# Optimization experiments

Hardware: AMD Instinct MI355X
Metric: run time of the kernel (lower is better)

The kernel has to match this reference:

```python
import jax, jax.numpy as jnp
import numpy as np

F = 128          # feature_dim
EMB = 128        # emb_dim[i] (all equal)
GH = 4           # gat heads per conv
GD = EMB // GH   # per-head conv out dim (is_concat=True)
AH = 8           # num_agg_heads
HID = EMB // AH  # n_hidden = 16
R = 3            # num_relations
L = 2            # num_layers
NC = 2           # num_classes
N = [100000, 50000, 25000]   # src frontier sizes per block (dst of block i = N[i+1])
E = [500000, 250000]         # edges per relation per block
SLOPE_CONV = 0.2             # DGL GATConv leaky slope
SLOPE_ACT = 0.01             # nn.LeakyReLU default

def lrelu(x, s):
    return jnp.where(x >= 0, x, s * x)

def setup_inputs() -> dict:
    key = jax.random.key(0)
    ks = iter(jax.random.split(key, 64))
    d = {}
    d['x'] = jax.random.normal(next(ks), (N[0], F), jnp.float32)
    d['src0'] = jax.random.randint(next(ks), (R, E[0]), 0, N[0], jnp.int32)
    d['dst0'] = jax.random.randint(next(ks), (R, E[0]), 0, N[1], jnp.int32)
    d['src1'] = jax.random.randint(next(ks), (R, E[1]), 0, N[1], jnp.int32)
    d['dst1'] = jax.random.randint(next(ks), (R, E[1]), 0, N[2], jnp.int32)
    def p(shape):
        return jax.random.normal(next(ks), shape, jnp.float32) * 0.05
    d['conv_W'] = p((L, R, F, EMB)); d['conv_al'] = p((L, R, GH, GD)); d['conv_ar'] = p((L, R, GH, GD))
    d['feat_W'] = p((L, F, EMB)); d['feat_b'] = p((L, EMB))
    d['relWl_W'] = p((L, F, EMB)); d['relWl_b'] = p((L, EMB))
    d['relWr_W'] = p((L, EMB, EMB)); d['relWr_b'] = p((L, EMB))
    d['relP_W'] = p((L, EMB, EMB)); d['relP_b'] = p((L, EMB))
    d['rela_W'] = p((L, HID)); d['rela_b'] = p((L,))
    d['proj_W'] = p((F, EMB)); d['proj_b'] = p((EMB,))
    d['hopWl_W'] = p((F, EMB)); d['hopWl_b'] = p((EMB,))
    d['hopWr_W'] = p((EMB, EMB)); d['hopWr_b'] = p((EMB,))
    d['hopP_W'] = p((EMB, EMB)); d['hopP_b'] = p((EMB,))
    d['hopa_W'] = p((HID,)); d['hopa_b'] = p(())
    d['lin_W'] = p((EMB, NC)); d['lin_b'] = p((NC,))
    return d

def gat_conv(x, n_dst, src, dst, W, al, ar):
    # x: [N_src, in]; dst features are x[:n_dst] (DGL block convention)
    h = (x @ W).reshape(-1, GH, GD)                 # [N_src, GH, GD]
    el = jnp.sum(h * al, -1)                        # [N_src, GH]
    er = jnp.sum(h * ar, -1)
    e = lrelu(el[src] + er[dst], SLOPE_CONV)        # [E, GH]
    emax = jax.ops.segment_max(e, dst, num_segments=n_dst)
    ee = jnp.exp(e - emax[dst])
    den = jax.ops.segment_sum(ee, dst, num_segments=n_dst)
    a = ee / den[dst]                               # edge softmax per dst node
    out = jax.ops.segment_sum(a[:, :, None] * h[src], dst, num_segments=n_dst)
    return out.reshape(n_dst, EMB)                  # is_concat reshape

def gated_attn(prev, feats, Wl, bl, Wr, br, Wp, bp, aW, ab):
    # prev: [n, in]; feats: [n, k, EMB]
    n, k, _ = feats.shape
    gl = (prev @ Wl + bl).reshape(n, AH, HID)
    gr = (feats @ Wr + br).reshape(n, k, AH, HID)
    z = lrelu(gl[:, None] + gr, SLOPE_ACT)
    e = jnp.einsum('nkah,h->nka', z, aW) + ab       # [n, k, AH]
    a = jax.nn.softmax(e, axis=1)                   # shift-invariant, matches e - amax
    v = (feats @ Wp + bp).reshape(n, k, AH, HID)
    return jnp.einsum('nka,nkah->nah', a, v).reshape(n, EMB)

def reference(x, src0, dst0, src1, dst1, conv_W, conv_al, conv_ar, feat_W, feat_b,
              relWl_W, relWl_b, relWr_W, relWr_b, relP_W, relP_b, rela_W, rela_b,
              proj_W, proj_b, hopWl_W, hopWl_b, hopWr_W, hopWr_b, hopP_W, hopP_b,
              hopa_W, hopa_b, lin_W, lin_b):
    n_out = N[L]
    layer_features = [x[:n_out] @ proj_W + proj_b]
    h = x
    srcs = [src0, src1]; dsts = [dst0, dst1]
    for i in range(L):
        n_dst = N[i + 1]
        feats = [lrelu(gat_conv(h, n_dst, srcs[i][j], dsts[i][j],
                                conv_W[i, j], conv_al[i, j], conv_ar[i, j]), SLOPE_ACT)
                 for j in range(R)]
        x_dst = h[:n_dst]
        feats.append(lrelu(x_dst @ feat_W[i] + feat_b[i], SLOPE_ACT))
        stacked = jnp.stack(feats, 1)               # [n_dst, R+1, EMB]
        h = lrelu(gated_attn(x_dst, stacked, relWl_W[i], relWl_b[i], relWr_W[i],
                             relWr_b[i], relP_W[i], relP_b[i], rela_W[i], rela_b[i]),
                  SLOPE_ACT)
        layer_features.append(h[:n_out])
    stacked = jnp.stack(layer_features, 1)          # [n_out, L+1, EMB]
    out = lrelu(gated_attn(x[:n_out], stacked, hopWl_W, hopWl_b, hopWr_W, hopWr_b,
                           hopP_W, hopP_b, hopa_W, hopa_b), SLOPE_ACT)
    return out @ lin_W + lin_b                      # [n_out, NC]
```

## Files before the change

### kernel.cpp

```cpp
#include <hip/hip_runtime.h>

#define N0 100000
#define N1 50000
#define N2 25000
#define E0 500000
#define E1 250000
#define N_TOT (3 * N1 + 3 * N2)
#define NE_ALL (3 * E0 + 3 * E1)
#define BNODE 512
#define NBUCK ((N_TOT + BNODE - 1) / BNODE)
#define BCAP 12288

typedef __attribute__((ext_vector_type(8))) short short8;
typedef __attribute__((ext_vector_type(4))) float f32x4;
typedef unsigned short ushort_t;
typedef unsigned int uint_t;

static __device__ __forceinline__ float lrelu(float x, float s) {
    return x >= 0.f ? x : s * x;
}

static __device__ __forceinline__ ushort_t f2bf(float f) {
    union { float f; uint_t u; } v; v.f = f;
    uint_t r = v.u + 0x7FFFu + ((v.u >> 16) & 1u);
    return (ushort_t)(r >> 16);
}

static __device__ __forceinline__ float bf_lo(uint_t u) {
    union { uint_t i; float f; } v; v.i = u << 16;
    return v.f;
}
static __device__ __forceinline__ float bf_hi(uint_t u) {
    union { uint_t i; float f; } v; v.i = u & 0xFFFF0000u;
    return v.f;
}

static __device__ __forceinline__ uint_t cvt2(float lo, float hi) {
    uint_t r;
    asm("v_cvt_pk_bf16_f32 %0, %1, %2" : "=v"(r) : "v"(lo), "v"(hi));
    return r;
}

template <int CT, int PLANES, int OUTMODE, int AB16, int OB16 = 0, int REPY = 0>
__global__ __launch_bounds__(256) void gemm_bf16(
    const void* __restrict__ A0, const void* __restrict__ A1,
    const void* __restrict__ A2, const void* __restrict__ A3,
    int nodes, const ushort_t* __restrict__ Bt, int cols,
    const float* __restrict__ biasA, const float* __restrict__ biasB,
    int colsplit, float slopeA, float slopeB,
    void* __restrict__ O1, int ld1, float* __restrict__ O2, int ld2,
    const float* __restrict__ glp, const float* __restrict__ aWp, int kreal,
    int repB = 0, int repO1 = 0, int repO2 = 0)
{
    constexpr int BCOLS = CT * 16;
    constexpr int NPANEL = (OUTMODE == 4) ? 2 : 1;
    constexpr int SCOLS = BCOLS * NPANEL;
    constexpr int CSTR = BCOLS + 4;
    constexpr int SH_B = SCOLS * 256;
    constexpr int SH_C = 64 * CSTR * 4 + ((OUTMODE == 4) ? 2048 : 0);
    constexpr int SHSZ = SH_B > SH_C ? SH_B : SH_C;
    constexpr int AELT = AB16 ? 2 : 4;
    __shared__ char sh[SHSZ];
    float* Cs = (float*)sh;

    const int Mrows = nodes * PLANES;
    const int row0 = blockIdx.x * 128;
    const int repy = REPY ? blockIdx.y : 0;
    const int cbase = REPY ? 0 : blockIdx.y * BCOLS;
    const ushort_t* Btp = Bt + (REPY ? (size_t)repy * repB : 0);
    ushort_t* O1p = (ushort_t*)O1 + (REPY ? (size_t)repy * repO1 : 0);
    float* O2p = O2 + (REPY ? (size_t)repy * repO2 : 0);
    const int tid = threadIdx.x;

    for (int u = tid; u < SCOLS * 16; u += 256) {
        int cl = u >> 4;
        int q = u & 15;
        int off = cl * 256 + q * 16;
        off ^= (cl & 7) << 4;
        int c;
        if (OUTMODE == 4)
            c = (cl < BCOLS) ? (cbase + cl) : (128 + cbase + (cl - BCOLS));
        else
            c = cbase + cl;
        uint4 d = make_uint4(0, 0, 0, 0);
        if (c < cols) d = *(const uint4*)(Btp + (size_t)c * 128 + q * 8);
        *(uint4*)(sh + off) = d;
    }
    __syncthreads();

    const int wv = tid >> 6;
    const int l = tid & 63;
    const int kg = l >> 4;
    const char* aptr[2];
    #pragma unroll
    for (int rt = 0; rt < 2; ++rt) {
        int rg = row0 + wv * 32 + rt * 16 + (l & 15);
        if (rg >= Mrows) rg = Mrows - 1;
        int node, pl;
        if (PLANES == 1) { node = rg; pl = 0; }
        else { node = rg / PLANES; pl = rg % PLANES; }
        const void* base = (pl == 0) ? A0 : (pl == 1) ? A1 : (pl == 2) ? A2 : A3;
        aptr[rt] = (const char*)base + ((size_t)node * 128 + kg * 8) * AELT;
    }

    f32x4 acc[2][CT];
    f32x4 accV[2][(OUTMODE == 4) ? CT : 1];
    #pragma unroll
    for (int a = 0; a < 2; ++a) {
        #pragma unroll
        for (int b = 0; b < CT; ++b)
            #pragma unroll
            for (int q = 0; q < 4; ++q) acc[a][b][q] = 0.f;
        if (OUTMODE == 4)
            #pragma unroll
            for (int b = 0; b < CT; ++b)
                #pragma unroll
                for (int q = 0; q < 4; ++q) accV[a][b][q] = 0.f;
    }

    #pragma unroll
    for (int kt = 0; kt < 4; ++kt) {
        short8 af[2];
        #pragma unroll
        for (int rt = 0; rt < 2; ++rt) {
            if (AB16) {
                af[rt] = *(const short8*)(aptr[rt] + (size_t)kt * 64);
            } else {
                const float4* p = (const float4*)(aptr[rt] + (size_t)kt * 128);
                float4 x0 = p[0];
                float4 x1 = p[1];
                union { uint_t u[4]; short8 s; } u;
                u.u[0] = cvt2(x0.x, x0.y);
                u.u[1] = cvt2(x0.z, x0.w);
                u.u[2] = cvt2(x1.x, x1.y);
                u.u[3] = cvt2(x1.z, x1.w);
                af[rt] = u.s;
            }
        }
        #pragma unroll
        for (int ct = 0; ct < CT; ++ct) {
            int off = ((ct * 16 + (l & 15)) * 256) + kt * 64 + (l >> 4) * 16;
            off ^= (l & 7) << 4;
            short8 bfr = *(const short8*)(sh + off);
            acc[0][ct] = __builtin_amdgcn_mfma_f32_16x16x32_bf16(af[0], bfr, acc[0][ct], 0, 0, 0);
            acc[1][ct] = __builtin_amdgcn_mfma_f32_16x16x32_bf16(af[1], bfr, acc[1][ct], 0, 0, 0);
            if (OUTMODE == 4) {
                int offv = ((BCOLS + ct * 16 + (l & 15)) * 256) + kt * 64 + (l >> 4) * 16;
                offv ^= (l & 7) << 4;
                short8 bfv = *(const short8*)(sh + offv);
                accV[0][ct] = __builtin_amdgcn_mfma_f32_16x16x32_bf16(af[0], bfv, accV[0][ct], 0, 0, 0);
                accV[1][ct] = __builtin_amdgcn_mfma_f32_16x16x32_bf16(af[1], bfv, accV[1][ct], 0, 0, 0);
            }
        }
    }

    if (OUTMODE == 4) {
        const int node0 = row0 >> 2;
        float* e_sh = (float*)(sh + 64 * CSTR * 4);
        float* w_sh = e_sh + 256;
        float4 aw0 = ((const float4*)aWp)[0];
        float4 aw1 = ((const float4*)aWp)[1];
        float4 aw2 = ((const float4*)aWp)[2];
        float4 aw3 = ((const float4*)aWp)[3];
        #pragma unroll
        for (int rt = 0; rt < 2; ++rt) {
            __syncthreads();
            #pragma unroll
            for (int ct = 0; ct < CT; ++ct) {
                int col = ct * 16 + (l & 15);
                float br_ = biasA[cbase + col];
                int lrow = wv * 16 + (l >> 4) * 4;
                #pragma unroll
                for (int j = 0; j < 4; ++j)
                    Cs[(lrow + j) * CSTR + col] = acc[rt][ct][j] + br_;
            }
            __syncthreads();
            {
                int row = tid >> 2, head = tid & 3;
                int rg = row0 + ((row >> 4) << 5) + rt * 16 + (row & 15);
                int node = rg >> 2;
                if (node > nodes - 1) node = nodes - 1;
                const float* zr = &Cs[row * CSTR + head * 16];
                const float* glr = glp + (size_t)node * 128 + cbase + head * 16;
                float4 c0 = *(const float4*)(zr);
                float4 c1 = *(const float4*)(zr + 4);
                float4 c2 = *(const float4*)(zr + 8);
                float4 c3 = *(const float4*)(zr + 12);
                float4 g0 = *(const float4*)(glr);
                float4 g1 = *(const float4*)(glr + 4);
                float4 g2 = *(const float4*)(glr + 8);
                float4 g3 = *(const float4*)(glr + 12);
                float e =
                    lrelu(c0.x + g0.x, 0.01f) * aw0.x + lrelu(c0.y + g0.y, 0.01f) * aw0.y +
                    lrelu(c0.z + g0.z, 0.01f) * aw0.z + lrelu(c0.w + g0.w, 0.01f) * aw0.w +
                    lrelu(c1.x + g1.x, 0.01f) * aw1.x + lrelu(c1.y + g1.y, 0.01f) * aw1.y +
                    lrelu(c1.z + g1.z, 0.01f) * aw1.z + lrelu(c1.w + g1.w, 0.01f) * aw1.w +
                    lrelu(c2.x + g2.x, 0.01f) * aw2.x + lrelu(c2.y + g2.y, 0.01f) * aw2.y +
                    lrelu(c2.z + g2.z, 0.01f) * aw2.z + lrelu(c2.w + g2.w, 0.01f) * aw2.w +
                    lrelu(c3.x + g3.x, 0.01f) * aw3.x + lrelu(c3.y + g3.y, 0.01f) * aw3.y +
                    lrelu(c3.z + g3.z, 0.01f) * aw3.z + lrelu(c3.w + g3.w, 0.01f) * aw3.w;
                e_sh[row * 4 + head] = e;
            }
            __syncthreads();
            if (tid < 64) {
                int q = tid >> 2, head = tid & 3;
                int rho0 = (q >> 2) * 16 + (q & 3) * 4;
                float e0 = e_sh[(rho0 + 0) * 4 + head];
                float e1 = e_sh[(rho0 + 1) * 4 + head];
                float e2 = e_sh[(rho0 + 2) * 4 + head];
                float e3 = (kreal == 4) ? e_sh[(rho0 + 3) * 4 + head] : -1e30f;
                float m = fmaxf(fmaxf(e0, e1), fmaxf(e2, e3));
                float x0 = __expf(e0 - m), x1 = __expf(e1 - m), x2 = __expf(e2 - m);
                float x3 = (kreal == 4) ? __expf(e3 - m) : 0.f;
                float inv = 1.f / (x0 + x1 + x2 + x3);
                w_sh[q * 16 + 0 + head] = x0 * inv;
                w_sh[q * 16 + 4 + head] = x1 * inv;
                w_sh[q * 16 + 8 + head] = x2 * inv;
                w_sh[q * 16 + 12 + head] = x3 * inv;
            }
            __syncthreads();
            #pragma unroll
            for (int ct = 0; ct < CT; ++ct) {
                int col = ct * 16 + (l & 15);
                float bp_ = biasB[cbase + col];
                int lrow = wv * 16 + (l >> 4) * 4;
                #pragma unroll
                for (int j = 0; j < 4; ++j)
                    Cs[(lrow + j) * CSTR + col] = accV[rt][ct][j] + bp_;
            }
            __syncthreads();
            {
                int nidx = tid >> 4;
                int c4 = tid & 15;
                int nl = rt * 4 + (nidx >> 2) * 8 + (nidx & 3);
                int gn = node0 + nl;
                if (gn < nodes) {
                    int head = c4 >> 2;
                    float4 o = make_float4(0.f, 0.f, 0.f, 0.f);
                    #pragma unroll
                    for (int k = 0; k < 4; ++k) {
                        int rho = (nidx >> 2) * 16 + (nidx & 3) * 4 + k;
                        float wk = w_sh[nidx * 16 + k * 4 + head];
                        float4 v4 = *(const float4*)&Cs[rho * CSTR + c4 * 4];
                        o.x += wk * v4.x; o.y += wk * v4.y;
                        o.z += wk * v4.z; o.w += wk * v4.w;
                    }
                    o.x = lrelu(o.x, 0.01f); o.y = lrelu(o.y, 0.01f);
                    o.z = lrelu(o.z, 0.01f); o.w = lrelu(o.w, 0.01f);
                    if (OB16) {
                        uint2 pk;
                        pk.x = cvt2(o.x, o.y);
                        pk.y = cvt2(o.z, o.w);
                        *(uint2*)((ushort_t*)O1 + (size_t)gn * 128 + cbase + c4 * 4) = pk;
                    } else {
                        *(float4*)((float*)O1 + (size_t)gn * 128 + cbase + c4 * 4) = o;
                    }
                }
            }
        }
        return;
    }

    #pragma unroll
    for (int rt = 0; rt < 2; ++rt) {
        __syncthreads();
        #pragma unroll
        for (int ct = 0; ct < CT; ++ct) {
            int c = cbase + ct * 16 + (l & 15);
            float bias_ = 0.f, slope_ = 1.f;
            if (c < colsplit) {
                if (biasA) bias_ = biasA[c];
                slope_ = slopeA;
            } else if (c < cols) {
                if (biasB) bias_ = biasB[c - colsplit];
                slope_ = slopeB;
            }
            int lrow = wv * 16 + (l >> 4) * 4;
            #pragma unroll
            for (int j = 0; j < 4; ++j) {
                float v = acc[rt][ct][j] + bias_;
                v = v >= 0.f ? v : v * slope_;
                Cs[(lrow + j) * CSTR + ct * 16 + (l & 15)] = v;
            }
        }
        __syncthreads();
        for (int i = tid; i < 64 * CT * 4; i += 256) {
            int rho = i / (CT * 4);
            int c4 = i - rho * (CT * 4);
            int col = c4 * 4;
            int gcol = cbase + col;
            int rg = row0 + rt * 16 + (rho >> 4) * 32 + (rho & 15);
            if (rg >= Mrows || gcol >= cols) continue;
            float4 v = *(const float4*)&Cs[rho * CSTR + col];
            if (gcol < 128) {
                uint2 pk;
                pk.x = cvt2(v.x, v.y);
                pk.y = cvt2(v.z, v.w);
                *(uint2*)(O1p + (size_t)rg * ld1 + gcol) = pk;
            } else {
                *(float4*)(O2p + (size_t)rg * ld2 + (gcol - 128)) = v;
            }
        }
    }
}

__global__ __launch_bounds__(256) void cvt_bf16(
    const float* __restrict__ in, ushort_t* __restrict__ out, int n8)
{
    int i = blockIdx.x * 256 + threadIdx.x;
    if (i >= n8) return;
    const float4* p = (const float4*)(in + (size_t)i * 8);
    float4 a = p[0], b = p[1];
    uint4 pk;
    pk.x = cvt2(a.x, a.y); pk.y = cvt2(a.z, a.w);
    pk.z = cvt2(b.x, b.y); pk.w = cvt2(b.z, b.w);
    *(uint4*)(out + (size_t)i * 8) = pk;
}

__global__ __launch_bounds__(128) void prep2(
    const float* __restrict__ Wa, const float* __restrict__ Wb, ushort_t* __restrict__ dst)
{
    int c = blockIdx.x, k = threadIdx.x;
    const float* W = (c < 128) ? Wa : Wb;
    int cc = c & 127;
    dst[c * 128 + k] = f2bf(W[k * 128 + cc]);
}

__global__ __launch_bounds__(128) void prep_conv(
    const float* __restrict__ W, const float* __restrict__ al, const float* __restrict__ ar,
    ushort_t* __restrict__ dst)
{
    int c = blockIdx.x, k = threadIdx.x;
    float v;
    if (c < 128) {
        v = W[k * 128 + c];
    } else {
        int idx = c - 128;
        int g = idx & 3;
        const float* a = (idx < 4) ? al : ar;
        float s = 0.f;
        for (int d = 0; d < 32; ++d) s += W[k * 128 + g * 32 + d] * a[g * 32 + d];
        v = s;
    }
    dst[c * 128 + k] = f2bf(v);
}

static __device__ __forceinline__ void edge_decode(
    int idx, const int* __restrict__ src0, const int* __restrict__ dst0,
    const int* __restrict__ src1, const int* __restrict__ dst1,
    int& src, int& gnode)
{
    if (idx < 3 * E0) {
        src = src0[idx];
        gnode = (idx / E0) * N1 + dst0[idx];
    } else {
        int k = idx - 3 * E0;
        src = src1[k];
        gnode = 3 * N1 + (k / E1) * N2 + dst1[k];
    }
}

__global__ __launch_bounds__(256) void bin_pass(
    const int* __restrict__ src0, const int* __restrict__ dst0,
    const int* __restrict__ src1, const int* __restrict__ dst1,
    int* __restrict__ bcur, uint_t* __restrict__ tmp)
{
    __shared__ int lcnt[512];
    __shared__ int lbase[512];
    const int tid = threadIdx.x;
    const int e0 = blockIdx.x * 4096;
    int sv[16], gv[16];
    for (int t = tid; t < 512; t += 256) lcnt[t] = 0;
    __syncthreads();
    #pragma unroll
    for (int i = 0; i < 16; ++i) {
        int idx = e0 + i * 256 + tid;
        if (idx < NE_ALL) {
            edge_decode(idx, src0, dst0, src1, dst1, sv[i], gv[i]);
            atomicAdd(&lcnt[gv[i] >> 9], 1);
        } else {
            gv[i] = -1; sv[i] = 0;
        }
    }
    __syncthreads();
    for (int t = tid; t < 512; t += 256) {
        int c = lcnt[t];
        lbase[t] = c ? atomicAdd(&bcur[t], c) : 0;
        lcnt[t] = 0;
    }
    __syncthreads();
    #pragma unroll
    for (int i = 0; i < 16; ++i) {
        if (gv[i] >= 0) {
            int b = gv[i] >> 9;
            int p = lbase[b] + atomicAdd(&lcnt[b], 1);
            if (p < BCAP)
                tmp[(size_t)b * BCAP + p] = (uint_t)((sv[i] << 9) | (gv[i] & 511));
        }
    }
}

__global__ __launch_bounds__(512) void bucket_scan(
    const int* __restrict__ bcur, int* __restrict__ bbase)
{
    __shared__ int s[512];
    int t = threadIdx.x;
    int v = (t < NBUCK) ? bcur[t] : 0;
    s[t] = v;
    __syncthreads();
    for (int off = 1; off < 512; off <<= 1) {
        int x = (t >= off) ? s[t - off] : 0;
        __syncthreads();
        s[t] += x;
        __syncthreads();
    }
    bbase[t] = s[t] - v;
}

__global__ __launch_bounds__(256) void build_pass(
    const int* __restrict__ bcur, const int* __restrict__ bbase,
    const uint_t* __restrict__ tmp, int* __restrict__ offs, int* __restrict__ csr)
{
    __shared__ int cnt[512];
    __shared__ int offl[512];
    __shared__ int ps[256];
    const int tid = threadIdx.x;
    const int b = blockIdx.x;
    int nE = bcur[b];
    if (nE > BCAP) nE = BCAP;
    const int base = bbase[b];
    const int node0 = b * BNODE;
    const uint_t* tp = tmp + (size_t)b * BCAP;

    for (int t = tid; t < 512; t += 256) cnt[t] = 0;
    __syncthreads();
    for (int i = tid; i < nE; i += 256)
        atomicAdd(&cnt[tp[i] & 511], 1);
    __syncthreads();
    int a0 = cnt[2 * tid], a1 = cnt[2 * tid + 1];
    ps[tid] = a0 + a1;
    __syncthreads();
    for (int off = 1; off < 256; off <<= 1) {
        int x = (tid >= off) ? ps[tid - off] : 0;
        __syncthreads();
        ps[tid] += x;
        __syncthreads();
    }
    int ex = ps[tid] - (a0 + a1);
    offl[2 * tid] = ex;
    offl[2 * tid + 1] = ex + a0;
    __syncthreads();
    for (int t = tid; t < BNODE; t += 256) {
        int gn = node0 + t;
        if (gn < N_TOT) offs[gn] = base + offl[t];
    }
    if (b == NBUCK - 1 && tid == 0) offs[N_TOT] = base + nE;
    for (int t = tid; t < 512; t += 256) cnt[t] = 0;
    __syncthreads();
    for (int i = tid; i < nE; i += 256) {
        uint_t pk = tp[i];
        int ld = pk & 511;
        int p = atomicAdd(&cnt[ld], 1);
        csr[base + offl[ld] + p] = (int)(pk >> 9);
    }
}

__global__ __launch_bounds__(256) void gat_gather6(
    const int* __restrict__ csrc, const int* __restrict__ offs,
    int base0, int nPerRep,
    const float* __restrict__ elr, int elrStride,
    const ushort_t* __restrict__ P, int pStride,
    ushort_t* __restrict__ out, int outStride)
{
    const int wv = threadIdx.x >> 6;
    const int g = blockIdx.x * 4 + wv;
    if (g >= 3 * nPerRep) return;
    const int rep = g / nPerRep;
    const int node = g - rep * nPerRep;
    const float* elrp = elr + (size_t)rep * elrStride;
    const ushort_t* Pp = P + (size_t)rep * pStride;
    ushort_t* outp = out + (size_t)rep * outStride;

    const int l = threadIdx.x & 63;
    const uint_t lane16 = l & 15;
    const int slot = l >> 4;
    const uint_t hg = lane16 >> 2;
    const int beg = offs[base0 + g], end = offs[base0 + g + 1];
    const float erg = elrp[(uint_t)node * 8u + 4u + hg];
    float den = 0.f;
    float a0 = 0.f, a1 = 0.f, a2 = 0.f, a3 = 0.f;
    float a4 = 0.f, a5 = 0.f, a6 = 0.f, a7 = 0.f;
    int i = beg + slot;
    for (; i + 4 < end; i += 8) {
        uint_t s0 = (uint_t)csrc[i];
        uint_t s1 = (uint_t)csrc[i + 4];
        float w0 = __expf(lrelu(elrp[s0 * 8u + hg] + erg, 0.2f));
        float w1 = __expf(lrelu(elrp[s1 * 8u + hg] + erg, 0.2f));
        uint4 d0 = *(const uint4*)(Pp + s0 * 128u + lane16 * 8u);
        uint4 d1 = *(const uint4*)(Pp + s1 * 128u + lane16 * 8u);
        den += w0 + w1;
        a0 += w0 * bf_lo(d0.x) + w1 * bf_lo(d1.x);
        a1 += w0 * bf_hi(d0.x) + w1 * bf_hi(d1.x);
        a2 += w0 * bf_lo(d0.y) + w1 * bf_lo(d1.y);
        a3 += w0 * bf_hi(d0.y) + w1 * bf_hi(d1.y);
        a4 += w0 * bf_lo(d0.z) + w1 * bf_lo(d1.z);
        a5 += w0 * bf_hi(d0.z) + w1 * bf_hi(d1.z);
        a6 += w0 * bf_lo(d0.w) + w1 * bf_lo(d1.w);
        a7 += w0 * bf_hi(d0.w) + w1 * bf_hi(d1.w);
    }
    if (i < end) {
        uint_t s0 = (uint_t)csrc[i];
        float w0 = __expf(lrelu(elrp[s0 * 8u + hg] + erg, 0.2f));
        uint4 d0 = *(const uint4*)(Pp + s0 * 128u + lane16 * 8u);
        den += w0;
        a0 += w0 * bf_lo(d0.x); a1 += w0 * bf_hi(d0.x);
        a2 += w0 * bf_lo(d0.y); a3 += w0 * bf_hi(d0.y);
        a4 += w0 * bf_lo(d0.z); a5 += w0 * bf_hi(d0.z);
        a6 += w0 * bf_lo(d0.w); a7 += w0 * bf_hi(d0.w);
    }
    #pragma unroll
    for (int m = 16; m <= 32; m <<= 1) {
        den += __shfl_xor(den, m);
        a0 += __shfl_xor(a0, m); a1 += __shfl_xor(a1, m);
        a2 += __shfl_xor(a2, m); a3 += __shfl_xor(a3, m);
        a4 += __shfl_xor(a4, m); a5 += __shfl_xor(a5, m);
        a6 += __shfl_xor(a6, m); a7 += __shfl_xor(a7, m);
    }
    if (slot == 0) {
        float inv = (end > beg) ? 1.f / den : 0.f;
        uint4 pk;
        pk.x = cvt2(lrelu(a0 * inv, 0.01f), lrelu(a1 * inv, 0.01f));
        pk.y = cvt2(lrelu(a2 * inv, 0.01f), lrelu(a3 * inv, 0.01f));
        pk.z = cvt2(lrelu(a4 * inv, 0.01f), lrelu(a5 * inv, 0.01f));
        pk.w = cvt2(lrelu(a6 * inv, 0.01f), lrelu(a7 * inv, 0.01f));
        *(uint4*)(outp + (uint_t)node * 128u + lane16 * 8u) = pk;
    }
}

__global__ __launch_bounds__(256) void lin_kernel(
    const float* __restrict__ H, const float* __restrict__ W,
    const float* __restrict__ b, float* __restrict__ out, int n)
{
    int idx = blockIdx.x * 256 + threadIdx.x;
    int node = idx >> 1, c = idx & 1;
    if (node >= n) return;
    float acc = 0.f;
    for (int k = 0; k < 128; ++k)
        acc += H[(size_t)node * 128 + k] * W[k * 2 + c];
    out[(size_t)node * 2 + c] = acc + b[c];
}

extern "C" void kernel_launch(void* const* d_in, const int* in_sizes, int n_in,
                              void* d_out, int out_size, void* d_ws, size_t ws_size,
                              hipStream_t stream)
{
    (void)in_sizes; (void)n_in; (void)out_size; (void)ws_size;
    const float* x       = (const float*)d_in[0];
    const int*   src0    = (const int*)d_in[1];
    const int*   dst0    = (const int*)d_in[2];
    const int*   src1    = (const int*)d_in[3];
    const int*   dst1    = (const int*)d_in[4];
    const float* conv_W  = (const float*)d_in[5];
    const float* conv_al = (const float*)d_in[6];
    const float* conv_ar = (const float*)d_in[7];
    const float* feat_W  = (const float*)d_in[8];
    const float* feat_b  = (const float*)d_in[9];
    const float* relWl_W = (const float*)d_in[10];
    const float* relWl_b = (const float*)d_in[11];
    const float* relWr_W = (const float*)d_in[12];
    const float* relWr_b = (const float*)d_in[13];
    const float* relP_W  = (const float*)d_in[14];
    const float* relP_b  = (const float*)d_in[15];
    const float* rela_W  = (const float*)d_in[16];
    const float* proj_W  = (const float*)d_in[18];
    const float* proj_b  = (const float*)d_in[19];
    const float* hopWl_W = (const float*)d_in[20];
    const float* hopWl_b = (const float*)d_in[21];
    const float* hopWr_W = (const float*)d_in[22];
    const float* hopWr_b = (const float*)d_in[23];
    const float* hopP_W  = (const float*)d_in[24];
    const float* hopP_b  = (const float*)d_in[25];
    const float* hopa_W  = (const float*)d_in[26];
    const float* lin_W   = (const float*)d_in[28];
    const float* lin_b   = (const float*)d_in[29];
    float* out = (float*)d_out;

    char* base = (char*)d_ws;
    size_t off = 0;
    auto alloc = [&](size_t bytes) -> void* {
        void* p = base + off;
        off += (bytes + 255) & ~(size_t)255;
        return p;
    };
    ushort_t* P     = (ushort_t*)alloc((size_t)3 * N0 * 128 * 2);
    float* elr      = (float*)alloc((size_t)3 * N0 * 8 * 4);
    ushort_t* x16   = (ushort_t*)alloc((size_t)N0 * 128 * 2);
    ushort_t* F     = (ushort_t*)alloc((size_t)3 * N1 * 128 * 2);
    ushort_t* F3    = (ushort_t*)alloc((size_t)N1 * 128 * 2);
    ushort_t* h1    = (ushort_t*)alloc((size_t)N1 * 128 * 2);
    ushort_t* h2    = (ushort_t*)alloc((size_t)N2 * 128 * 2);
    float* glbuf    = (float*)alloc((size_t)N1 * 128 * 4);
    float* glhop    = (float*)alloc((size_t)N2 * 128 * 4);
    int*   csr_all  = (int*)alloc((size_t)NE_ALL * 4);
    int*   offs     = (int*)alloc((size_t)(N_TOT + 1) * 4);
    int*   bcur     = (int*)alloc(512 * 4);
    int*   bbase    = (int*)alloc(512 * 4);
    ushort_t* pconvA = (ushort_t*)alloc((size_t)6 * 136 * 128 * 2);
    ushort_t* p2L0 = (ushort_t*)alloc(256 * 128 * 2);
    ushort_t* p2L1 = (ushort_t*)alloc(256 * 128 * 2);
    ushort_t* pE   = (ushort_t*)alloc(256 * 128 * 2);
    ushort_t* pF0  = (ushort_t*)alloc(256 * 128 * 2);
    ushort_t* pF1  = (ushort_t*)alloc(256 * 128 * 2);
    ushort_t* pG   = (ushort_t*)alloc(256 * 128 * 2);

    ushort_t* F0 = F;
    ushort_t* F1 = F + (size_t)N1 * 128;
    ushort_t* F2 = F + (size_t)2 * N1 * 128;
    ushort_t* hopp0 = F0;
    float* hout  = glbuf;
    uint_t* tmp  = (uint_t*)F;

    for (int i = 0; i < 6; ++i)
        prep_conv<<<136, 128, 0, stream>>>(conv_W + (size_t)i * 16384,
                                           conv_al + (size_t)i * 128,
                                           conv_ar + (size_t)i * 128,
                                           pconvA + (size_t)i * 136 * 128);
    prep2<<<256, 128, 0, stream>>>(feat_W, relWl_W, p2L0);
    prep2<<<256, 128, 0, stream>>>(feat_W + 16384, relWl_W + 16384, p2L1);
    prep2<<<256, 128, 0, stream>>>(proj_W, hopWl_W, pE);
    prep2<<<256, 128, 0, stream>>>(relWr_W, relP_W, pF0);
    prep2<<<256, 128, 0, stream>>>(relWr_W + 16384, relP_W + 16384, pF1);
    prep2<<<256, 128, 0, stream>>>(hopWr_W, hopP_W, pG);
    cvt_bf16<<<(N0 * 16 + 255) / 256, 256, 0, stream>>>(x, x16, N0 * 16);

    hipMemsetAsync(bcur, 0, 512 * 4, stream);
    bin_pass<<<(NE_ALL + 4095) / 4096, 256, 0, stream>>>(src0, dst0, src1, dst1, bcur, tmp);
    bucket_scan<<<1, 512, 0, stream>>>(bcur, bbase);
    build_pass<<<NBUCK, 256, 0, stream>>>(bcur, bbase, tmp, offs, csr_all);

    gemm_bf16<9, 1, 1, 1, 0, 1><<<dim3((N0 + 127) / 128, 3), 256, 0, stream>>>(
        x16, x16, x16, x16, N0, pconvA, 136, nullptr, nullptr, 128, 1.f, 1.f,
        P, 128, elr, 8, nullptr, nullptr, 0,
        136 * 128, N0 * 128, N0 * 8);
    gat_gather6<<<(3 * N1 + 3) / 4, 256, 0, stream>>>(
        csr_all, offs, 0, N1, elr, N0 * 8, P, N0 * 128, F, N1 * 128);
    gemm_bf16<8, 1, 1, 1><<<dim3((N1 + 127) / 128, 2), 256, 0, stream>>>(
        x16, x16, x16, x16, N1, p2L0, 256, feat_b, relWl_b, 128, 0.01f, 1.f,
        F3, 128, glbuf, 128, nullptr, nullptr, 0);
    gemm_bf16<4, 4, 4, 1, 1><<<dim3((N1 * 4 + 127) / 128, 2), 256, 0, stream>>>(
        F0, F1, F2, F3, N1, pF0, 256, relWr_b, relP_b, 128, 1.f, 1.f,
        h1, 128, nullptr, 0, glbuf, rela_W, 4);

    gemm_bf16<9, 1, 1, 1, 0, 1><<<dim3((N1 + 127) / 128, 3), 256, 0, stream>>>(
        h1, h1, h1, h1, N1, pconvA + (size_t)3 * 136 * 128, 136,
        nullptr, nullptr, 128, 1.f, 1.f,
        P, 128, elr, 8, nullptr, nullptr, 0,
        136 * 128, N0 * 128, N0 * 8);
    gat_gather6<<<(3 * N2 + 3) / 4, 256, 0, stream>>>(
        csr_all, offs, 3 * N1, N2, elr, N0 * 8, P, N0 * 128, F, N1 * 128);
    gemm_bf16<8, 1, 1, 1><<<dim3((N2 + 127) / 128, 2), 256, 0, stream>>>(
        h1, h1, h1, h1, N2, p2L1, 256, feat_b + 128, relWl_b + 128, 128, 0.01f, 1.f,
        F3, 128, glbuf, 128, nullptr, nullptr, 0);
    gemm_bf16<4, 4, 4, 1, 1><<<dim3((N2 * 4 + 127) / 128, 2), 256, 0, stream>>>(
        F0, F1, F2, F3, N2, pF1, 256, relWr_b + 128, relP_b + 128, 128, 1.f, 1.f,
        h2, 128, nullptr, 0, glbuf, rela_W + 16, 4);

    gemm_bf16<8, 1, 1, 1><<<dim3((N2 + 127) / 128, 2), 256, 0, stream>>>(
        x16, x16, x16, x16, N2, pE, 256, proj_b, hopWl_b, 128, 1.f, 1.f,
        hopp0, 128, glhop, 128, nullptr, nullptr, 0);

    gemm_bf16<4, 4, 4, 1, 0><<<dim3((N2 * 4 + 127) / 128, 2), 256, 0, stream>>>(
        hopp0, h1, h2, hopp0, N2, pG, 256, hopWr_b, hopP_b, 128, 1.f, 1.f,
        hout, 128, nullptr, 0, glhop, hopa_W, 3);

    lin_kernel<<<(N2 * 2 + 255) / 256, 256, 0, stream>>>(hout, lin_W, lin_b, out, N2);
}
```

Before: 463.8 us.

## Merge prep launches, fold bucket scan into build pass, unroll gather by four

Thirteen weight-prep and input-cast launches are merged into one prep_all kernel dispatched by block index. The separate single-block bucket scan is removed; each build_pass block now recomputes the prefix sum over bucket counts itself. The GAT gather loop gets a four-edge unrolled path ahead of the two-edge loop to expose more memory-level parallelism. Together these cut launch count and gap overhead, at the cost of redundant scans per block and more registers in the gather.

```diff
diff --git a/kernel.cpp b/kernel.cpp
--- a/kernel.cpp
+++ b/kernel.cpp
@@ -304,45 +304,50 @@
     }
 }
 
-__global__ __launch_bounds__(256) void cvt_bf16(
-    const float* __restrict__ in, ushort_t* __restrict__ out, int n8)
+struct P2Job { const float* Wa; const float* Wb; ushort_t* dst; };
+struct PrepArgs {
+    const float* conv_W; const float* conv_al; const float* conv_ar;
+    ushort_t* pconvA;
+    P2Job j[6];
+    const float* x; ushort_t* x16;
+};
+
+__global__ __launch_bounds__(128) void prep_all(PrepArgs pa)
 {
-    int i = blockIdx.x * 256 + threadIdx.x;
-    if (i >= n8) return;
-    const float4* p = (const float4*)(in + (size_t)i * 8);
-    float4 a = p[0], b = p[1];
-    uint4 pk;
-    pk.x = cvt2(a.x, a.y); pk.y = cvt2(a.z, a.w);
-    pk.z = cvt2(b.x, b.y); pk.w = cvt2(b.z, b.w);
-    *(uint4*)(out + (size_t)i * 8) = pk;
-}
-
-__global__ __launch_bounds__(128) void prep2(
-    const float* __restrict__ Wa, const float* __restrict__ Wb, ushort_t* __restrict__ dst)
-{
-    int c = blockIdx.x, k = threadIdx.x;
-    const float* W = (c < 128) ? Wa : Wb;
-    int cc = c & 127;
-    dst[c * 128 + k] = f2bf(W[k * 128 + cc]);
-}
-
-__global__ __launch_bounds__(128) void prep_conv(
-    const float* __restrict__ W, const float* __restrict__ al, const float* __restrict__ ar,
-    ushort_t* __restrict__ dst)
-{
-    int c = blockIdx.x, k = threadIdx.x;
-    float v;
-    if (c < 128) {
-        v = W[k * 128 + c];
+    const int bid = blockIdx.x;
+    const int k = threadIdx.x;
+    if (bid < 816) {
+        int jj = bid / 136, c = bid - jj * 136;
+        const float* W = pa.conv_W + (size_t)jj * 16384;
+        float v;
+        if (c < 128) {
+            v = W[k * 128 + c];
+        } else {
+            int idx = c - 128;
+            int g = idx & 3;
+            const float* a = ((idx < 4) ? pa.conv_al : pa.conv_ar) + jj * 128;
+            float s = 0.f;
+            for (int d = 0; d < 32; ++d) s += W[k * 128 + g * 32 + d] * a[g * 32 + d];
+            v = s;
+        }
+        pa.pconvA[(size_t)jj * 136 * 128 + c * 128 + k] = f2bf(v);
+    } else if (bid < 816 + 1536) {
+        int b2 = bid - 816;
+        int jj = b2 >> 8, c = b2 & 255;
+        const float* W = (c < 128) ? pa.j[jj].Wa : pa.j[jj].Wb;
+        int cc = c & 127;
+        pa.j[jj].dst[c * 128 + k] = f2bf(W[k * 128 + cc]);
     } else {
-        int idx = c - 128;
-        int g = idx & 3;
-        const float* a = (idx < 4) ? al : ar;
-        float s = 0.f;
-        for (int d = 0; d < 32; ++d) s += W[k * 128 + g * 32 + d] * a[g * 32 + d];
-        v = s;
-    }
-    dst[c * 128 + k] = f2bf(v);
+        int idx = (bid - 2352) * 128 + k;
+        if (idx < N0 * 16) {
+            const float4* p = (const float4*)(pa.x + (size_t)idx * 8);
+            float4 a = p[0], b = p[1];
+            uint4 pk;
+            pk.x = cvt2(a.x, a.y); pk.y = cvt2(a.z, a.w);
+            pk.z = cvt2(b.x, b.y); pk.w = cvt2(b.z, b.w);
+            *(uint4*)(pa.x16 + (size_t)idx * 8) = pk;
+        }
+    }
 }
 
 static __device__ __forceinline__ void edge_decode(
@@ -400,45 +405,20 @@
     }
 }
 
-__global__ __launch_bounds__(512) void bucket_scan(
-    const int* __restrict__ bcur, int* __restrict__ bbase)
-{
-    __shared__ int s[512];
-    int t = threadIdx.x;
-    int v = (t < NBUCK) ? bcur[t] : 0;
-    s[t] = v;
-    __syncthreads();
-    for (int off = 1; off < 512; off <<= 1) {
-        int x = (t >= off) ? s[t - off] : 0;
-        __syncthreads();
-        s[t] += x;
-        __syncthreads();
-    }
-    bbase[t] = s[t] - v;
-}
-
-__global__ __launch_bounds__(256) void build_pass(
-    const int* __restrict__ bcur, const int* __restrict__ bbase,
-    const uint_t* __restrict__ tmp, int* __restrict__ offs, int* __restrict__ csr)
+__global__ __launch_bounds__(256) void build_pass2(
+    const int* __restrict__ bcur, const uint_t* __restrict__ tmp,
+    int* __restrict__ offs, int* __restrict__ csr)
 {
     __shared__ int cnt[512];
     __shared__ int offl[512];
     __shared__ int ps[256];
+    __shared__ int pbase[512];
     const int tid = threadIdx.x;
     const int b = blockIdx.x;
-    int nE = bcur[b];
-    if (nE > BCAP) nE = BCAP;
-    const int base = bbase[b];
-    const int node0 = b * BNODE;
-    const uint_t* tp = tmp + (size_t)b * BCAP;
-
-    for (int t = tid; t < 512; t += 256) cnt[t] = 0;
-    __syncthreads();
-    for (int i = tid; i < nE; i += 256)
-        atomicAdd(&cnt[tp[i] & 511], 1);
-    __syncthreads();
-    int a0 = cnt[2 * tid], a1 = cnt[2 * tid + 1];
-    ps[tid] = a0 + a1;
+
+    int v0 = (2 * tid < NBUCK) ? bcur[2 * tid] : 0;
+    int v1 = (2 * tid + 1 < NBUCK) ? bcur[2 * tid + 1] : 0;
+    ps[tid] = v0 + v1;
     __syncthreads();
     for (int off = 1; off < 256; off <<= 1) {
         int x = (tid >= off) ? ps[tid - off] : 0;
@@ -446,6 +426,33 @@
         ps[tid] += x;
         __syncthreads();
     }
+    {
+        int ex = ps[tid] - (v0 + v1);
+        pbase[2 * tid] = ex;
+        pbase[2 * tid + 1] = ex + v0;
+    }
+    __syncthreads();
+    const int base = pbase[b];
+
+    int nE = bcur[b];
+    if (nE > BCAP) nE = BCAP;
+    const int node0 = b * BNODE;
+    const uint_t* tp = tmp + (size_t)b * BCAP;
+
+    for (int t = tid; t < 512; t += 256) cnt[t] = 0;
+    __syncthreads();
+    for (int i = tid; i < nE; i += 256)
+        atomicAdd(&cnt[tp[i] & 511], 1);
+    __syncthreads();
+    int a0 = cnt[2 * tid], a1 = cnt[2 * tid + 1];
+    ps[tid] = a0 + a1;
+    __syncthreads();
+    for (int off = 1; off < 256; off <<= 1) {
+        int x = (tid >= off) ? ps[tid - off] : 0;
+        __syncthreads();
+        ps[tid] += x;
+        __syncthreads();
+    }
     int ex = ps[tid] - (a0 + a1);
     offl[2 * tid] = ex;
     offl[2 * tid + 1] = ex + a0;
@@ -465,7 +472,7 @@
     }
 }
 
-__global__ __launch_bounds__(256) void gat_gather6(
+__global__ __launch_bounds__(256) void gat_gather7(
     const int* __restrict__ csrc, const int* __restrict__ offs,
     int base0, int nPerRep,
     const float* __restrict__ elr, int elrStride,
@@ -491,6 +498,29 @@
     float a0 = 0.f, a1 = 0.f, a2 = 0.f, a3 = 0.f;
     float a4 = 0.f, a5 = 0.f, a6 = 0.f, a7 = 0.f;
     int i = beg + slot;
+    for (; i + 12 < end; i += 16) {
+        uint_t s0 = (uint_t)csrc[i];
+        uint_t s1 = (uint_t)csrc[i + 4];
+        uint_t s2 = (uint_t)csrc[i + 8];
+        uint_t s3 = (uint_t)csrc[i + 12];
+        float w0 = __expf(lrelu(elrp[s0 * 8u + hg] + erg, 0.2f));
+        float w1 = __expf(lrelu(elrp[s1 * 8u + hg] + erg, 0.2f));
+        float w2 = __expf(lrelu(elrp[s2 * 8u + hg] + erg, 0.2f));
+        float w3 = __expf(lrelu(elrp[s3 * 8u + hg] + erg, 0.2f));
+        uint4 d0 = *(const uint4*)(Pp + s0 * 128u + lane16 * 8u);
+        uint4 d1 = *(const uint4*)(Pp + s1 * 128u + lane16 * 8u);
+        uint4 d2 = *(const uint4*)(Pp + s2 * 128u + lane16 * 8u);
+        uint4 d3 = *(const uint4*)(Pp + s3 * 128u + lane16 * 8u);
+        den += (w0 + w1) + (w2 + w3);
+        a0 += w0 * bf_lo(d0.x) + w1 * bf_lo(d1.x) + w2 * bf_lo(d2.x) + w3 * bf_lo(d3.x);
+        a1 += w0 * bf_hi(d0.x) + w1 * bf_hi(d1.x) + w2 * bf_hi(d2.x) + w3 * bf_hi(d3.x);
+        a2 += w0 * bf_lo(d0.y) + w1 * bf_lo(d1.y) + w2 * bf_lo(d2.y) + w3 * bf_lo(d3.y);
+        a3 += w0 * bf_hi(d0.y) + w1 * bf_hi(d1.y) + w2 * bf_hi(d2.y) + w3 * bf_hi(d3.y);
+        a4 += w0 * bf_lo(d0.z) + w1 * bf_lo(d1.z) + w2 * bf_lo(d2.z) + w3 * bf_lo(d3.z);
+        a5 += w0 * bf_hi(d0.z) + w1 * bf_hi(d1.z) + w2 * bf_hi(d2.z) + w3 * bf_hi(d3.z);
+        a6 += w0 * bf_lo(d0.w) + w1 * bf_lo(d1.w) + w2 * bf_lo(d2.w) + w3 * bf_lo(d3.w);
+        a7 += w0 * bf_hi(d0.w) + w1 * bf_hi(d1.w) + w2 * bf_hi(d2.w) + w3 * bf_hi(d3.w);
+    }
     for (; i + 4 < end; i += 8) {
         uint_t s0 = (uint_t)csrc[i];
         uint_t s1 = (uint_t)csrc[i + 4];
@@ -604,7 +634,6 @@
     int*   csr_all  = (int*)alloc((size_t)NE_ALL * 4);
     int*   offs     = (int*)alloc((size_t)(N_TOT + 1) * 4);
     int*   bcur     = (int*)alloc(512 * 4);
-    int*   bbase    = (int*)alloc(512 * 4);
     ushort_t* pconvA = (ushort_t*)alloc((size_t)6 * 136 * 128 * 2);
     ushort_t* p2L0 = (ushort_t*)alloc(256 * 128 * 2);
     ushort_t* p2L1 = (ushort_t*)alloc(256 * 128 * 2);
@@ -620,29 +649,26 @@
     float* hout  = glbuf;
     uint_t* tmp  = (uint_t*)F;
 
-    for (int i = 0; i < 6; ++i)
-        prep_conv<<<136, 128, 0, stream>>>(conv_W + (size_t)i * 16384,
-                                           conv_al + (size_t)i * 128,
-                                           conv_ar + (size_t)i * 128,
-                                           pconvA + (size_t)i * 136 * 128);
-    prep2<<<256, 128, 0, stream>>>(feat_W, relWl_W, p2L0);
-    prep2<<<256, 128, 0, stream>>>(feat_W + 16384, relWl_W + 16384, p2L1);
-    prep2<<<256, 128, 0, stream>>>(proj_W, hopWl_W, pE);
-    prep2<<<256, 128, 0, stream>>>(relWr_W, relP_W, pF0);
-    prep2<<<256, 128, 0, stream>>>(relWr_W + 16384, relP_W + 16384, pF1);
-    prep2<<<256, 128, 0, stream>>>(hopWr_W, hopP_W, pG);
-    cvt_bf16<<<(N0 * 16 + 255) / 256, 256, 0, stream>>>(x, x16, N0 * 16);
+    PrepArgs pa;
+    pa.conv_W = conv_W; pa.conv_al = conv_al; pa.conv_ar = conv_ar; pa.pconvA = pconvA;
+    pa.j[0] = {feat_W, relWl_W, p2L0};
+    pa.j[1] = {feat_W + 16384, relWl_W + 16384, p2L1};
+    pa.j[2] = {proj_W, hopWl_W, pE};
+    pa.j[3] = {relWr_W, relP_W, pF0};
+    pa.j[4] = {relWr_W + 16384, relP_W + 16384, pF1};
+    pa.j[5] = {hopWr_W, hopP_W, pG};
+    pa.x = x; pa.x16 = x16;
+    prep_all<<<816 + 1536 + 12500, 128, 0, stream>>>(pa);
 
     hipMemsetAsync(bcur, 0, 512 * 4, stream);
     bin_pass<<<(NE_ALL + 4095) / 4096, 256, 0, stream>>>(src0, dst0, src1, dst1, bcur, tmp);
-    bucket_scan<<<1, 512, 0, stream>>>(bcur, bbase);
-    build_pass<<<NBUCK, 256, 0, stream>>>(bcur, bbase, tmp, offs, csr_all);
+    build_pass2<<<NBUCK, 256, 0, stream>>>(bcur, tmp, offs, csr_all);
 
     gemm_bf16<9, 1, 1, 1, 0, 1><<<dim3((N0 + 127) / 128, 3), 256, 0, stream>>>(
         x16, x16, x16, x16, N0, pconvA, 136, nullptr, nullptr, 128, 1.f, 1.f,
         P, 128, elr, 8, nullptr, nullptr, 0,
         136 * 128, N0 * 128, N0 * 8);
-    gat_gather6<<<(3 * N1 + 3) / 4, 256, 0, stream>>>(
+    gat_gather7<<<(3 * N1 + 3) / 4, 256, 0, stream>>>(
         csr_all, offs, 0, N1, elr, N0 * 8, P, N0 * 128, F, N1 * 128);
     gemm_bf16<8, 1, 1, 1><<<dim3((N1 + 127) / 128, 2), 256, 0, stream>>>(
         x16, x16, x16, x16, N1, p2L0, 256, feat_b, relWl_b, 128, 0.01f, 1.f,
@@ -656,7 +682,7 @@
         nullptr, nullptr, 128, 1.f, 1.f,
         P, 128, elr, 8, nullptr, nullptr, 0,
         136 * 128, N0 * 128, N0 * 8);
-    gat_gather6<<<(3 * N2 + 3) / 4, 256, 0, stream>>>(
+    gat_gather7<<<(3 * N2 + 3) / 4, 256, 0, stream>>>(
         csr_all, offs, 3 * N1, N2, elr, N0 * 8, P, N0 * 128, F, N1 * 128);
     gemm_bf16<8, 1, 1, 1><<<dim3((N2 + 127) / 128, 2), 256, 0, stream>>>(
         h1, h1, h1, h1, N2, p2L1, 256, feat_b + 128, relWl_b + 128, 128, 0.01f, 1.f,
```

Result: faster. 429.3 us (-7.4%).
